# Performance work log

Measured on AMD Instinct MI355X. Metric: run time of the kernel, lower is better.

Reference implementation:

```python
import jax, jax.numpy as jnp
import numpy as np

B, S, D = 2, 2048, 2048
H = 16
NOPE, ROPE, VH = 128, 64, 128
QR, KVR = 512, 512
EPS = 1e-6


def _rmsnorm(x, w):
    return x * jax.lax.rsqrt(jnp.mean(x * x, axis=-1, keepdims=True) + EPS) * w


def _rope(t, freqs_cis):
    # t: (B, h, S, ROPE); freqs_cis: (S, ROPE//2, 2) as (cos, sin)
    b, h, s, d = t.shape
    t2 = t.reshape(b, h, s, d // 2, 2)
    cos = freqs_cis[:, :, 0][None, None]  # (1,1,S,ROPE//2)
    sin = freqs_cis[:, :, 1][None, None]
    x0, x1 = t2[..., 0], t2[..., 1]
    r0 = x0 * cos - x1 * sin
    r1 = x0 * sin + x1 * cos
    return jnp.stack([r0, r1], axis=-1).reshape(b, h, s, d)


def setup_inputs() -> dict:
    key = jax.random.key(0)
    ks = jax.random.split(key, 11)
    def init(k, out_dim, in_dim):
        return jax.random.normal(k, (out_dim, in_dim), jnp.float32) * (1.0 / np.sqrt(in_dim))
    x = jax.random.normal(ks[0], (B, S, D), jnp.float32)
    half = ROPE // 2
    inv = 1.0 / (10000.0 ** (np.arange(half, dtype=np.float64) / half))
    ang = np.outer(np.arange(S), inv)
    freqs_cis = jnp.asarray(np.stack([np.cos(ang), np.sin(ang)], axis=-1), jnp.float32)  # (S, half, 2)
    mask = jnp.ones((S, S), dtype=bool)  # unused (is_causal=True in original)
    return {
        "x": x,
        "mask": mask,
        "freqs_cis": freqs_cis,
        "w_cq": init(ks[1], QR, D),
        "w_qnorm": jnp.ones((QR,), jnp.float32),
        "w_dqn": init(ks[2], H * NOPE, QR),
        "w_dqr": init(ks[3], H * ROPE, QR),
        "w_ckv": init(ks[4], KVR, D),
        "w_kvnorm": jnp.ones((KVR,), jnp.float32),
        "w_dkn": init(ks[5], H * NOPE, KVR),
        "w_dv": init(ks[6], H * VH, KVR),
        "w_krope": init(ks[7], ROPE, D),
        "w_proj": init(ks[8], D, H * VH),
    }


def reference(x, mask, freqs_cis, w_cq, w_qnorm, w_dqn, w_dqr, w_ckv, w_kvnorm, w_dkn, w_dv, w_krope, w_proj):
    b, s, _ = x.shape
    # Q path: compress -> RMSNorm -> decompress (nope, rope)
    cq = jnp.einsum('bsd,rd->bsr', x, w_cq)
    nq = _rmsnorm(cq, w_qnorm)
    q_nope = jnp.einsum('bsr,er->bse', nq, w_dqn).reshape(b, s, H, NOPE).transpose(0, 2, 1, 3)
    q_rope = jnp.einsum('bsr,er->bse', nq, w_dqr).reshape(b, s, H, ROPE).transpose(0, 2, 1, 3)
    # KV path
    ckv = jnp.einsum('bsd,rd->bsr', x, w_ckv)
    nkv = _rmsnorm(ckv, w_kvnorm)
    k_nope = jnp.einsum('bsr,er->bse', nkv, w_dkn).reshape(b, s, H, NOPE).transpose(0, 2, 1, 3)
    value = jnp.einsum('bsr,er->bse', nkv, w_dv).reshape(b, s, H, VH).transpose(0, 2, 1, 3)
    # shared single-head rope key, scaled by 1/num_heads
    k_rope = jnp.einsum('bsd,ed->bse', x, w_krope).reshape(b, s, 1, ROPE).transpose(0, 2, 1, 3) / H
    # partial RoPE
    q_rope = _rope(q_rope, freqs_cis)
    k_rope = _rope(k_rope, freqs_cis)
    # recombine nope|rope
    q = jnp.concatenate([q_nope, q_rope], axis=-1)  # (B,H,S,NOPE+ROPE)
    k = jnp.concatenate([k_nope, jnp.broadcast_to(k_rope, (b, H, s, ROPE))], axis=-1)
    # causal SDPA
    scale = 1.0 / np.sqrt(NOPE + ROPE)
    scores = jnp.einsum('bhqd,bhkd->bhqk', q, k) * scale
    causal = jnp.tril(jnp.ones((s, s), dtype=bool))
    scores = jnp.where(causal[None, None], scores, -jnp.inf)
    attn = jax.nn.softmax(scores, axis=-1)
    out = jnp.einsum('bhqk,bhkv->bhqv', attn, value)  # (B,H,S,VH)
    out = out.transpose(0, 2, 1, 3).reshape(b, s, H * VH)
    return jnp.einsum('bse,de->bsd', out, w_proj)
```

## Files before the change

### kernel.cpp

```cpp
#include <hip/hip_runtime.h>
#include <hip/hip_bf16.h>


typedef __attribute__((ext_vector_type(8))) short s8v;
typedef __attribute__((ext_vector_type(4))) float f4v;

#define DEV static __device__ __forceinline__

DEV ushort f2b(float f) {
  __hip_bfloat16 h = __float2bfloat16(f);
  return *reinterpret_cast<ushort*>(&h);
}
DEV float b2f(ushort u) {
  __hip_bfloat16 h = *reinterpret_cast<__hip_bfloat16*>(&u);
  return __bfloat162float(h);
}
DEV f4v mfma16(s8v a, s8v b, f4v c) {
  return __builtin_amdgcn_mfma_f32_16x16x32_bf16(a, b, c, 0, 0, 0);
}
DEV void gload16(const ushort* g, ushort* l) {
  __builtin_amdgcn_global_load_lds((const __attribute__((address_space(1))) void*)g,
                                   (__attribute__((address_space(3))) void*)l, 16, 0, 0);
}
DEV void barrier_raw() {
  __builtin_amdgcn_sched_barrier(0);
  __builtin_amdgcn_s_barrier();
  __builtin_amdgcn_sched_barrier(0);
}

struct CastSeg { const float* src; ushort* dst; int n4; int blk0; };
struct CastTab { CastSeg seg[10]; };

__global__ __launch_bounds__(256) void cast_all_kernel(CastTab t) {
  int b = blockIdx.x;
  int si = 0;
#pragma unroll
  for (int i = 1; i < 10; ++i) si = (b >= t.seg[i].blk0) ? i : si;
  int i4 = (b - t.seg[si].blk0) * 256 + threadIdx.x;
  if (i4 >= t.seg[si].n4) return;
  ushort4 o;
  if (t.seg[si].src) {
    float4 v = reinterpret_cast<const float4*>(t.seg[si].src)[i4];
    o.x = f2b(v.x); o.y = f2b(v.y); o.z = f2b(v.z); o.w = f2b(v.w);
  } else {
    o = ushort4{0, 0, 0, 0};
  }
  reinterpret_cast<ushort4*>(t.seg[si].dst)[i4] = o;
}

template <bool BF16OUT>
DEV void gemm_core(const ushort* __restrict__ A, const ushort* __restrict__ B,
                   void* __restrict__ C, int N, int K, int row0, int col0,
                   ushort* a_lds0, ushort* a_lds1, ushort* b_lds0, ushort* b_lds1) {
  const int tid = threadIdx.x;
  const int lane = tid & 63, wv = tid >> 6;
  const int wm = wv >> 1, wn = wv & 1;
  const int l15 = lane & 15, l4 = lane >> 4;
  const int srow = lane >> 2;
  const int scol = (lane & 3) * 8;
  ushort* a_lds[2] = {a_lds0, a_lds1};
  ushort* b_lds[2] = {b_lds0, b_lds1};

  f4v acc[4][4];
#pragma unroll
  for (int i = 0; i < 4; ++i)
#pragma unroll
    for (int j = 0; j < 4; ++j) acc[i][j] = f4v{0.f, 0.f, 0.f, 0.f};

  auto stage = [&](int k0, int bsel) {
#pragma unroll
    for (int i = 0; i < 2; ++i) {
      int s = wv * 2 + i;
      gload16(&A[(size_t)(row0 + s * 16 + srow) * K + k0 + scol], &a_lds[bsel][s * 512]);
      gload16(&B[(size_t)(col0 + s * 16 + srow) * K + k0 + scol], &b_lds[bsel][s * 512]);
    }
  };

  stage(0, 0);
  int cur = 0;
  for (int k0 = 0; k0 < K; k0 += 32) {
    __syncthreads();
    if (k0 + 32 < K) stage(k0 + 32, cur ^ 1);
    s8v af[4], bfr[4];
#pragma unroll
    for (int mi = 0; mi < 4; ++mi)
      af[mi] = *reinterpret_cast<const s8v*>(&a_lds[cur][(wm * 64 + mi * 16 + l15) * 32 + 8 * l4]);
#pragma unroll
    for (int ni = 0; ni < 4; ++ni)
      bfr[ni] = *reinterpret_cast<const s8v*>(&b_lds[cur][(wn * 64 + ni * 16 + l15) * 32 + 8 * l4]);
#pragma unroll
    for (int mi = 0; mi < 4; ++mi)
#pragma unroll
      for (int ni = 0; ni < 4; ++ni) acc[mi][ni] = mfma16(af[mi], bfr[ni], acc[mi][ni]);
    cur ^= 1;
  }

#pragma unroll
  for (int mi = 0; mi < 4; ++mi)
#pragma unroll
    for (int ni = 0; ni < 4; ++ni)
#pragma unroll
      for (int j = 0; j < 4; ++j) {
        int r = row0 + wm * 64 + mi * 16 + l4 * 4 + j;
        int cl = col0 + wn * 64 + ni * 16 + l15;
        if (BF16OUT)
          reinterpret_cast<ushort*>(C)[(size_t)r * N + cl] = f2b(acc[mi][ni][j]);
        else
          reinterpret_cast<float*>(C)[(size_t)r * N + cl] = acc[mi][ni][j];
      }
}

template <bool BF16OUT>
__global__ __launch_bounds__(256) void gemm_bt(const ushort* __restrict__ A,
                                               const ushort* __restrict__ B,
                                               void* __restrict__ C, int N, int K) {
  __shared__ ushort a0[128 * 32], a1[128 * 32], b0[128 * 32], b1[128 * 32];
  gemm_core<BF16OUT>(A, B, C, N, K, blockIdx.x * 128, blockIdx.y * 128, a0, a1, b0, b1);
}

__global__ __launch_bounds__(256) void gemm2_dual(const ushort* __restrict__ nq,
                                                  const ushort* __restrict__ w2q,
                                                  ushort* __restrict__ g2q,
                                                  const ushort* __restrict__ nkv,
                                                  const ushort* __restrict__ w2kv,
                                                  ushort* __restrict__ g2kv) {
  __shared__ ushort a0[128 * 32], a1[128 * 32], b0[128 * 32], b1[128 * 32];
  int by = blockIdx.y;
  if (by < 24)
    gemm_core<true>(nq, w2q, g2q, 3072, 512, blockIdx.x * 128, by * 128, a0, a1, b0, b1);
  else
    gemm_core<true>(nkv, w2kv, g2kv, 4096, 512, blockIdx.x * 128, (by - 24) * 128, a0, a1, b0, b1);
}

__global__ __launch_bounds__(256) void norm_rope1_kernel(
    const float* __restrict__ g1, const float* __restrict__ wq, const float* __restrict__ wkv,
    const float* __restrict__ freqs, ushort* __restrict__ nq, ushort* __restrict__ nkv,
    ushort* __restrict__ kro) {
  const int m = blockIdx.x;
  const int s = m & 2047;
  const int tid = threadIdx.x;
  __shared__ float red[4];
  const float* row = g1 + (size_t)m * 1152;

  float v0 = row[tid], v1 = row[tid + 256];
  float ss = v0 * v0 + v1 * v1;
#pragma unroll
  for (int off = 32; off > 0; off >>= 1) ss += __shfl_down(ss, off);
  if ((tid & 63) == 0) red[tid >> 6] = ss;
  __syncthreads();
  float r = rsqrtf((red[0] + red[1] + red[2] + red[3]) * (1.0f / 512.0f) + 1e-6f);
  nq[(size_t)m * 512 + tid] = f2b(v0 * r * wq[tid]);
  nq[(size_t)m * 512 + tid + 256] = f2b(v1 * r * wq[tid + 256]);

  float u0 = row[512 + tid], u1 = row[512 + tid + 256];
  float ss2 = u0 * u0 + u1 * u1;
#pragma unroll
  for (int off = 32; off > 0; off >>= 1) ss2 += __shfl_down(ss2, off);
  __syncthreads();
  if ((tid & 63) == 0) red[tid >> 6] = ss2;
  __syncthreads();
  float r2 = rsqrtf((red[0] + red[1] + red[2] + red[3]) * (1.0f / 512.0f) + 1e-6f);
  nkv[(size_t)m * 512 + tid] = f2b(u0 * r2 * wkv[tid]);
  nkv[(size_t)m * 512 + tid + 256] = f2b(u1 * r2 * wkv[tid + 256]);

  if (tid < 32) {
    float x0 = row[1024 + 2 * tid], x1 = row[1024 + 2 * tid + 1];
    float c = freqs[s * 64 + 2 * tid], sn = freqs[s * 64 + 2 * tid + 1];
    kro[(size_t)m * 64 + 2 * tid] = f2b((x0 * c - x1 * sn) * (1.0f / 16.0f));
    kro[(size_t)m * 64 + 2 * tid + 1] = f2b((x0 * sn + x1 * c) * (1.0f / 16.0f));
  }
}

__global__ __launch_bounds__(256) void misc_fused_kernel(ushort* __restrict__ g2q,
                                                         const float* __restrict__ freqs,
                                                         const ushort* __restrict__ g2kv,
                                                         ushort* __restrict__ vT) {
  const int tid = threadIdx.x;
  if (blockIdx.x < 2048) {
    int blk = blockIdx.x;
    int bh = blk >> 6;
    int rem = blk & 63;
    int st = rem >> 1, dt = rem & 1;
    int b = bh >> 4, h = bh & 15;
    __shared__ ushort t[64][72];
#pragma unroll
    for (int it = 0; it < 2; ++it) {
      int c = tid + it * 256;
      int sl = c >> 3, cc = (c & 7) * 8;
      *reinterpret_cast<uint4*>(&t[sl][cc]) = *reinterpret_cast<const uint4*>(
          &g2kv[(size_t)(b * 2048 + st * 64 + sl) * 4096 + 2048 + h * 128 + dt * 64 + cc]);
    }
    __syncthreads();
#pragma unroll
    for (int it = 0; it < 2; ++it) {
      int c = tid + it * 256;
      int dl = c >> 3, cc = (c & 7) * 8;
      ushort tmp[8];
#pragma unroll
      for (int e = 0; e < 8; ++e) tmp[e] = t[cc + e][dl];
      *reinterpret_cast<uint4*>(&vT[(size_t)(bh * 128 + dt * 64 + dl) * 2048 + st * 64 + cc]) =
          *reinterpret_cast<uint4*>(tmp);
    }
  } else {
    int idx = (blockIdx.x - 2048) * 256 + tid;
    int m = idx >> 9;
    int rem = idx & 511;
    int h = rem >> 5, j = rem & 31;
    int s = m & 2047;
    size_t base = (size_t)m * 3072 + 2048 + h * 64 + 2 * j;
    ushort2 pr = *reinterpret_cast<ushort2*>(&g2q[base]);
    float x0 = b2f(pr.x), x1 = b2f(pr.y);
    float c = freqs[s * 64 + 2 * j], sn = freqs[s * 64 + 2 * j + 1];
    ushort2 o;
    o.x = f2b(x0 * c - x1 * sn);
    o.y = f2b(x0 * sn + x1 * c);
    *reinterpret_cast<ushort2*>(&g2q[base]) = o;
  }
}

__global__ __launch_bounds__(512, 4) void attn_kernel(const ushort* __restrict__ q,
                                                      const ushort* __restrict__ knope,
                                                      const ushort* __restrict__ kro,
                                                      const ushort* __restrict__ vT,
                                                      ushort* __restrict__ out) {
  const int p = blockIdx.x;
  const int a = (p >> 5) & 7;
  const int qt = (p < 256) ? (15 - a) : a;
  const int bh = p & 31;
  const int b = bh >> 4, h = bh & 15;
  const int tid = threadIdx.x, lane = tid & 63, w = tid >> 6;
  const int l15 = lane & 15, l4 = lane >> 4;

  __shared__ ushort kbuf[2][64 * 192];
  __shared__ ushort vbuf[128 * 64];

  s8v qf[6];
  {
    const size_t qbase = (size_t)(b * 2048 + qt * 128 + w * 16 + l15) * 3072;
#pragma unroll
    for (int kc = 0; kc < 4; ++kc)
      qf[kc] = *reinterpret_cast<const s8v*>(&q[qbase + h * 128 + kc * 32 + 8 * l4]);
#pragma unroll
    for (int kc = 4; kc < 6; ++kc)
      qf[kc] = *reinterpret_cast<const s8v*>(&q[qbase + 2048 + h * 64 + (kc - 4) * 32 + 8 * l4]);
  }

  f4v oacc[8];
#pragma unroll
  for (int i = 0; i < 8; ++i) oacc[i] = f4v{0.f, 0.f, 0.f, 0.f};
  float m_r = -INFINITY, l_r = 0.f;
  const float sc2 = 0.07216878364870323f * 1.44269504f;
  const int nkt = 2 * qt + 2;
  const int kbase = b * 2048;
  const int myq = qt * 128 + w * 16 + l15;

  auto stageK = [&](int kt, int bsel) {
    const int krow0 = kbase + kt * 64;
#pragma unroll
    for (int i = 0; i < 3; ++i) {
      int s = w * 3 + i;
      int pp = s * 1024 + lane * 16;
      int row = pp / 384;
      int col = ((pp ^ ((row & 7) << 4)) - row * 384) >> 1;
      const ushort* src = (col < 128)
          ? &knope[(size_t)(krow0 + row) * 4096 + h * 128 + col]
          : &kro[(size_t)(krow0 + row) * 64 + (col - 128)];
      gload16(src, &kbuf[bsel][s * 512]);
    }
  };
  auto stageV = [&](int kt) {
#pragma unroll
    for (int i = 0; i < 2; ++i) {
      int s = w * 2 + i;
      int pp = s * 1024 + lane * 16;
      int d = pp >> 7;
      int key = ((pp ^ ((d & 7) << 4)) & 127) >> 1;
      gload16(&vT[(size_t)(bh * 128 + d) * 2048 + kt * 64 + key], &vbuf[s * 512]);
    }
  };

  stageK(0, 0);
  int cur = 0;
  for (int kt = 0; kt < nkt; ++kt) {
    asm volatile("s_waitcnt vmcnt(0)" ::: "memory");
    barrier_raw();
    stageV(kt);
    if (kt + 1 < nkt) stageK(kt + 1, cur ^ 1);
    const char* kb = (const char*)kbuf[cur];

    f4v sacc[4];
    __builtin_amdgcn_s_setprio(1);
#pragma unroll
    for (int nb = 0; nb < 4; ++nb) {
      sacc[nb] = f4v{0.f, 0.f, 0.f, 0.f};
      const int row = nb * 16 + l15;
      const int sw = (row & 7) << 4;
#pragma unroll
      for (int kc = 0; kc < 6; ++kc) {
        s8v kf = *reinterpret_cast<const s8v*>(kb + row * 384 + ((kc * 64 + l4 * 16) ^ sw));
        sacc[nb] = mfma16(kf, qf[kc], sacc[nb]);
      }
    }
    __builtin_amdgcn_s_setprio(0);

#pragma unroll
    for (int nb = 0; nb < 4; ++nb) {
      int key = kt * 64 + nb * 16 + 4 * l4;
#pragma unroll
      for (int j = 0; j < 4; ++j) {
        float sv = sacc[nb][j] * sc2;
        if (kt >= 2 * qt && key + j > myq) sv = -INFINITY;
        sacc[nb][j] = sv;
      }
    }
    float mx = sacc[0][0];
#pragma unroll
    for (int nb = 0; nb < 4; ++nb)
#pragma unroll
      for (int j = 0; j < 4; ++j) mx = fmaxf(mx, sacc[nb][j]);
    mx = fmaxf(mx, __shfl_xor(mx, 16));
    mx = fmaxf(mx, __shfl_xor(mx, 32));

    if (!__all(mx - m_r <= 8.0f)) {
      float mnew = fmaxf(m_r, mx);
      float al = exp2f(m_r - mnew);
      m_r = mnew;
      l_r *= al;
      float alj[4];
#pragma unroll
      for (int j = 0; j < 4; ++j) alj[j] = __shfl(al, 4 * l4 + j);
#pragma unroll
      for (int nv = 0; nv < 8; ++nv)
#pragma unroll
        for (int j = 0; j < 4; ++j) oacc[nv][j] *= alj[j];
    }
    float rs = 0.f;
#pragma unroll
    for (int nb = 0; nb < 4; ++nb)
#pragma unroll
      for (int j = 0; j < 4; ++j) {
        float pv = exp2f(sacc[nb][j] - m_r);
        sacc[nb][j] = pv;
        rs += pv;
      }
    rs += __shfl_xor(rs, 16);
    rs += __shfl_xor(rs, 32);
    l_r += rs;

    uint pkE[4], pkO[4];
#pragma unroll
    for (int nb = 0; nb < 4; ++nb) {
      pkE[nb] = ((uint)f2b(sacc[nb][1]) << 16) | f2b(sacc[nb][0]);
      pkO[nb] = ((uint)f2b(sacc[nb][3]) << 16) | f2b(sacc[nb][2]);
    }
    const int hi2 = l4 >> 1;
    const int sbase = l15 + 16 * (2 * (l4 & 1));
    union PF { uint u[4]; s8v v; } pf0, pf1;
#pragma unroll
    for (int t = 0; t < 4; ++t) {
      int src = sbase + 16 * (t >> 1);
      uint wa0 = __shfl((t & 1) ? pkO[0] : pkE[0], src);
      uint wb0 = __shfl((t & 1) ? pkO[1] : pkE[1], src);
      pf0.u[t] = hi2 ? wb0 : wa0;
      uint wa1 = __shfl((t & 1) ? pkO[2] : pkE[2], src);
      uint wb1 = __shfl((t & 1) ? pkO[3] : pkE[3], src);
      pf1.u[t] = hi2 ? wb1 : wa1;
    }

    if (kt + 1 < nkt) {
      asm volatile("s_waitcnt vmcnt(3)" ::: "memory");
    } else {
      asm volatile("s_waitcnt vmcnt(0)" ::: "memory");
    }
    barrier_raw();

    const char* vb = (const char*)vbuf;
    __builtin_amdgcn_s_setprio(1);
#pragma unroll
    for (int kc2 = 0; kc2 < 2; ++kc2) {
      s8v pfr = kc2 ? pf1.v : pf0.v;
#pragma unroll
      for (int nv = 0; nv < 8; ++nv) {
        const int d = nv * 16 + l15;
        s8v vf = *reinterpret_cast<const s8v*>(vb + d * 128 + ((kc2 * 64 + l4 * 16) ^ ((d & 7) << 4)));
        oacc[nv] = mfma16(pfr, vf, oacc[nv]);
      }
    }
    __builtin_amdgcn_s_setprio(0);
    cur ^= 1;
  }

  float invl = 1.0f / l_r;
  float invj[4];
#pragma unroll
  for (int j = 0; j < 4; ++j) invj[j] = __shfl(invl, 4 * l4 + j);
#pragma unroll
  for (int j = 0; j < 4; ++j) {
    int m = b * 2048 + qt * 128 + w * 16 + 4 * l4 + j;
#pragma unroll
    for (int nv = 0; nv < 8; ++nv)
      out[(size_t)m * 2048 + h * 128 + nv * 16 + l15] = f2b(oacc[nv][j] * invj[j]);
  }
}

extern "C" void kernel_launch(void* const* d_in, const int* in_sizes, int n_in,
                              void* d_out, int out_size, void* d_ws, size_t ws_size,
                              hipStream_t stream) {
  const float* x       = (const float*)d_in[0];
  const float* freqs   = (const float*)d_in[2];
  const float* w_cq    = (const float*)d_in[3];
  const float* w_qnorm = (const float*)d_in[4];
  const float* w_dqn   = (const float*)d_in[5];
  const float* w_dqr   = (const float*)d_in[6];
  const float* w_ckv   = (const float*)d_in[7];
  const float* w_kvnorm= (const float*)d_in[8];
  const float* w_dkn   = (const float*)d_in[9];
  const float* w_dv    = (const float*)d_in[10];
  const float* w_krope = (const float*)d_in[11];
  const float* w_proj  = (const float*)d_in[12];
  float* out = (float*)d_out;

  char* ws = (char*)d_ws;
  const size_t MB = 1ull << 20;
  ushort* g2kv = (ushort*)(ws + 0);
  float*  g1   = (float*) (ws + 0);
  ushort* g2q  = (ushort*)(ws + 32 * MB);
  ushort* xbf  = (ushort*)(ws + 32 * MB);
  ushort* w1   = (ushort*)(ws + 48 * MB);
  ushort* vT   = (ushort*)(ws + 56 * MB);
  ushort* nq   = (ushort*)(ws + 56 * MB);
  ushort* nkv  = (ushort*)(ws + 60 * MB);
  ushort* w2q  = (ushort*)(ws + 64 * MB);
  ushort* w2kv = (ushort*)(ws + 67 * MB);
  ushort* att  = (ushort*)(ws + 72 * MB);
  ushort* wpj  = (ushort*)(ws + 88 * MB);
  ushort* kro  = (ushort*)(ws + 96 * MB);

  CastTab t;
  const float* srcs[10] = {x, w_cq, w_ckv, w_krope, nullptr,
                           w_dqn, w_dqr, w_dkn, w_dv, w_proj};
  ushort* dsts[10] = {xbf, w1, w1 + 512 * 2048, w1 + 1024 * 2048, w1 + 1088 * 2048,
                      w2q, w2q + 2048 * 512, w2kv, w2kv + 2048 * 512, wpj};
  int ns[10] = {4096 * 2048, 512 * 2048, 512 * 2048, 64 * 2048, 64 * 2048,
                2048 * 512, 1024 * 512, 2048 * 512, 2048 * 512, 2048 * 2048};
  int blk = 0;
  for (int i = 0; i < 10; ++i) {
    t.seg[i].src = srcs[i];
    t.seg[i].dst = dsts[i];
    t.seg[i].n4 = ns[i] / 4;
    t.seg[i].blk0 = blk;
    blk += (ns[i] / 4 + 255) / 256;
  }
  cast_all_kernel<<<blk, 256, 0, stream>>>(t);

  gemm_bt<false><<<dim3(32, 9), 256, 0, stream>>>(xbf, w1, g1, 1152, 2048);
  norm_rope1_kernel<<<4096, 256, 0, stream>>>(g1, w_qnorm, w_kvnorm, freqs, nq, nkv, kro);
  gemm2_dual<<<dim3(32, 56), 256, 0, stream>>>(nq, w2q, g2q, nkv, w2kv, g2kv);
  misc_fused_kernel<<<2048 + 8192, 256, 0, stream>>>(g2q, freqs, g2kv, vT);
  attn_kernel<<<512, 512, 0, stream>>>(g2q, g2kv, kro, vT, att);
  gemm_bt<false><<<dim3(32, 16), 256, 0, stream>>>(att, wpj, out, 2048, 2048);
}
```

Measured before the change: 461.8 us.

## Balance causal attention work by splitting heavy query tiles across blocks with merge

Each block now processes exactly 17 KV tiles. It pairs a heavy query tile (8+pi) with a light one (7-pi), and the heavy tile's KV range is split between two blocks that write partial O/m/l, which a new merge kernel combines. V staging is also double-buffered, which removes the mid-iteration barrier. The aim is to remove the load imbalance from causal masking and the extra sync per tile. The cost is fp32 partial traffic (kept in the output buffer as scratch), an extra kernel launch, and more shared memory.

Result: no change. 468.0 us (+1.3%).

```diff
diff --git a/kernel.cpp b/kernel.cpp
--- a/kernel.cpp
+++ b/kernel.cpp
@@ -218,24 +218,35 @@
   }
 }
 
+#define MINIT -3.0e4f
 __global__ __launch_bounds__(512, 4) void attn_kernel(const ushort* __restrict__ q,
                                                       const ushort* __restrict__ knope,
                                                       const ushort* __restrict__ kro,
                                                       const ushort* __restrict__ vT,
-                                                      ushort* __restrict__ out) {
-  const int p = blockIdx.x;
-  const int a = (p >> 5) & 7;
-  const int qt = (p < 256) ? (15 - a) : a;
-  const int bh = p & 31;
+                                                      ushort* __restrict__ out,
+                                                      float* __restrict__ opart,
+                                                      float* __restrict__ mlbuf) {
+  const int g = blockIdx.x;
+  const int pi = g >> 6;
+  const int half = (g >> 5) & 1;
+  const int bh = g & 31;
+  const int qt_h = 8 + pi, qt_l = 7 - pi;
   const int b = bh >> 4, h = bh & 15;
   const int tid = threadIdx.x, lane = tid & 63, w = tid >> 6;
   const int l15 = lane & 15, l4 = lane >> 4;
 
   __shared__ ushort kbuf[2][64 * 192];
-  __shared__ ushort vbuf[128 * 64];
+  __shared__ ushort vbuf[2][128 * 64];
+
+  const int n1 = half ? (2 * qt_h - 15) : 17;
+  const int kvA0 = half ? 17 : 0;
+  const int NJ = 17;
+
+  auto jobQt = [&](int i) { return (i < n1) ? qt_h : qt_l; };
+  auto jobKv = [&](int i) { return (i < n1) ? (kvA0 + i) : (i - n1); };
 
   s8v qf[6];
-  {
+  auto loadQ = [&](int qt) {
     const size_t qbase = (size_t)(b * 2048 + qt * 128 + w * 16 + l15) * 3072;
 #pragma unroll
     for (int kc = 0; kc < 4; ++kc)
@@ -243,19 +254,21 @@
 #pragma unroll
     for (int kc = 4; kc < 6; ++kc)
       qf[kc] = *reinterpret_cast<const s8v*>(&q[qbase + 2048 + h * 64 + (kc - 4) * 32 + 8 * l4]);
-  }
+  };
 
   f4v oacc[8];
-#pragma unroll
-  for (int i = 0; i < 8; ++i) oacc[i] = f4v{0.f, 0.f, 0.f, 0.f};
-  float m_r = -INFINITY, l_r = 0.f;
+  float m_r, l_r;
+  auto resetS = [&]() {
+#pragma unroll
+    for (int i = 0; i < 8; ++i) oacc[i] = f4v{0.f, 0.f, 0.f, 0.f};
+    m_r = MINIT; l_r = 0.f;
+  };
+
   const float sc2 = 0.07216878364870323f * 1.44269504f;
-  const int nkt = 2 * qt + 2;
   const int kbase = b * 2048;
-  const int myq = qt * 128 + w * 16 + l15;
-
-  auto stageK = [&](int kt, int bsel) {
-    const int krow0 = kbase + kt * 64;
+
+  auto stageK = [&](int kv, int bsel) {
+    const int krow0 = kbase + kv * 64;
 #pragma unroll
     for (int i = 0; i < 3; ++i) {
       int s = w * 3 + i;
@@ -268,25 +281,64 @@
       gload16(src, &kbuf[bsel][s * 512]);
     }
   };
-  auto stageV = [&](int kt) {
+  auto stageV = [&](int kv, int bsel) {
 #pragma unroll
     for (int i = 0; i < 2; ++i) {
       int s = w * 2 + i;
       int pp = s * 1024 + lane * 16;
       int d = pp >> 7;
       int key = ((pp ^ ((d & 7) << 4)) & 127) >> 1;
-      gload16(&vT[(size_t)(bh * 128 + d) * 2048 + kt * 64 + key], &vbuf[s * 512]);
-    }
-  };
-
-  stageK(0, 0);
-  int cur = 0;
-  for (int kt = 0; kt < nkt; ++kt) {
+      gload16(&vT[(size_t)(bh * 128 + d) * 2048 + kv * 64 + key], &vbuf[bsel][s * 512]);
+    }
+  };
+
+  auto writePartial = [&](int part) {
+    float* Op = opart + (((size_t)(pi * 32 + bh) * 2 + part) << 14);
+#pragma unroll
+    for (int j = 0; j < 4; ++j)
+#pragma unroll
+      for (int nv = 0; nv < 8; ++nv)
+        Op[(w * 16 + 4 * l4 + j) * 128 + nv * 16 + l15] = oacc[nv][j];
+    if (l4 == 0) {
+      float* mlp = mlbuf + ((pi * 32 + bh) * 2 + part) * 256 + (w * 16 + l15) * 2;
+      mlp[0] = m_r; mlp[1] = l_r;
+    }
+  };
+  auto writeFinal = [&](int qt) {
+    float invl = 1.0f / l_r;
+    float invj[4];
+#pragma unroll
+    for (int j = 0; j < 4; ++j) invj[j] = __shfl(invl, 4 * l4 + j);
+#pragma unroll
+    for (int j = 0; j < 4; ++j) {
+      int m = b * 2048 + qt * 128 + w * 16 + 4 * l4 + j;
+#pragma unroll
+      for (int nv = 0; nv < 8; ++nv)
+        out[(size_t)m * 2048 + h * 128 + nv * 16 + l15] = f2b(oacc[nv][j] * invj[j]);
+    }
+  };
+
+  loadQ(jobQt(0));
+  resetS();
+  stageK(jobKv(0), 0);
+  stageV(jobKv(0), 0);
+
+  for (int i = 0; i < NJ; ++i) {
     asm volatile("s_waitcnt vmcnt(0)" ::: "memory");
     barrier_raw();
-    stageV(kt);
-    if (kt + 1 < nkt) stageK(kt + 1, cur ^ 1);
-    const char* kb = (const char*)kbuf[cur];
+    if (i + 1 < NJ) {
+      stageV(jobKv(i + 1), (i + 1) & 1);
+      stageK(jobKv(i + 1), (i + 1) & 1);
+    }
+    if (half && i == n1) {
+      writePartial(1);
+      resetS();
+      loadQ(qt_l);
+    }
+    const int qt = jobQt(i), kv = jobKv(i);
+    const int myq = qt * 128 + w * 16 + l15;
+    const char* kb = (const char*)kbuf[i & 1];
+    const char* vb = (const char*)vbuf[i & 1];
 
     f4v sacc[4];
     __builtin_amdgcn_s_setprio(1);
@@ -305,11 +357,11 @@
 
 #pragma unroll
     for (int nb = 0; nb < 4; ++nb) {
-      int key = kt * 64 + nb * 16 + 4 * l4;
+      int key = kv * 64 + nb * 16 + 4 * l4;
 #pragma unroll
       for (int j = 0; j < 4; ++j) {
         float sv = sacc[nb][j] * sc2;
-        if (kt >= 2 * qt && key + j > myq) sv = -INFINITY;
+        if (kv >= 2 * qt && key + j > myq) sv = -INFINITY;
         sacc[nb][j] = sv;
       }
     }
@@ -367,14 +419,6 @@
       pf1.u[t] = hi2 ? wb1 : wa1;
     }
 
-    if (kt + 1 < nkt) {
-      asm volatile("s_waitcnt vmcnt(3)" ::: "memory");
-    } else {
-      asm volatile("s_waitcnt vmcnt(0)" ::: "memory");
-    }
-    barrier_raw();
-
-    const char* vb = (const char*)vbuf;
     __builtin_amdgcn_s_setprio(1);
 #pragma unroll
     for (int kc2 = 0; kc2 < 2; ++kc2) {
@@ -387,19 +431,41 @@
       }
     }
     __builtin_amdgcn_s_setprio(0);
-    cur ^= 1;
-  }
-
-  float invl = 1.0f / l_r;
-  float invj[4];
-#pragma unroll
-  for (int j = 0; j < 4; ++j) invj[j] = __shfl(invl, 4 * l4 + j);
-#pragma unroll
-  for (int j = 0; j < 4; ++j) {
-    int m = b * 2048 + qt * 128 + w * 16 + 4 * l4 + j;
-#pragma unroll
-    for (int nv = 0; nv < 8; ++nv)
-      out[(size_t)m * 2048 + h * 128 + nv * 16 + l15] = f2b(oacc[nv][j] * invj[j]);
+  }
+
+  if (half == 0) writePartial(0);
+  else writeFinal(qt_l);
+}
+
+__global__ __launch_bounds__(256) void merge_kernel(const float* __restrict__ opart,
+                                                    const float* __restrict__ mlbuf,
+                                                    ushort* __restrict__ att) {
+  const int g = blockIdx.x;
+  const int pi = g >> 5, bh = g & 31;
+  const int qt = 8 + pi, b = bh >> 4, h = bh & 15;
+  const int t = threadIdx.x;
+  const int r = t >> 1, c0 = (t & 1) * 64;
+
+  const int pb = (pi * 32 + bh) * 2;
+  float m0 = mlbuf[pb * 256 + r * 2], l0 = mlbuf[pb * 256 + r * 2 + 1];
+  float m1 = mlbuf[(pb + 1) * 256 + r * 2], l1 = mlbuf[(pb + 1) * 256 + r * 2 + 1];
+  float m = fmaxf(m0, m1);
+  float a0 = exp2f(m0 - m), a1 = exp2f(m1 - m);
+  float inv = 1.0f / (l0 * a0 + l1 * a1);
+
+  const float* O0 = opart + ((size_t)pb << 14) + r * 128 + c0;
+  const float* O1 = opart + ((size_t)(pb + 1) << 14) + r * 128 + c0;
+  ushort* dst = att + (size_t)(b * 2048 + qt * 128 + r) * 2048 + h * 128 + c0;
+#pragma unroll
+  for (int d = 0; d < 64; d += 4) {
+    float4 v0 = *reinterpret_cast<const float4*>(O0 + d);
+    float4 v1 = *reinterpret_cast<const float4*>(O1 + d);
+    ushort4 o;
+    o.x = f2b((v0.x * a0 + v1.x * a1) * inv);
+    o.y = f2b((v0.y * a0 + v1.y * a1) * inv);
+    o.z = f2b((v0.z * a0 + v1.z * a1) * inv);
+    o.w = f2b((v0.w * a0 + v1.w * a1) * inv);
+    *reinterpret_cast<ushort4*>(dst + d) = o;
   }
 }
 
@@ -435,6 +501,8 @@
   ushort* att  = (ushort*)(ws + 72 * MB);
   ushort* wpj  = (ushort*)(ws + 88 * MB);
   ushort* kro  = (ushort*)(ws + 96 * MB);
+  float*  mlb  = (float*) (ws + 97 * MB);
+  float*  opart= out;
 
   CastTab t;
   const float* srcs[10] = {x, w_cq, w_ckv, w_krope, nullptr,
@@ -457,6 +525,7 @@
   norm_rope1_kernel<<<4096, 256, 0, stream>>>(g1, w_qnorm, w_kvnorm, freqs, nq, nkv, kro);
   gemm2_dual<<<dim3(32, 56), 256, 0, stream>>>(nq, w2q, g2q, nkv, w2kv, g2kv);
   misc_fused_kernel<<<2048 + 8192, 256, 0, stream>>>(g2q, freqs, g2kv, vT);
-  attn_kernel<<<512, 512, 0, stream>>>(g2q, g2kv, kro, vT, att);
+  attn_kernel<<<512, 512, 0, stream>>>(g2q, g2kv, kro, vT, att, opart, mlb);
+  merge_kernel<<<256, 256, 0, stream>>>(opart, mlb, att);
   gemm_bt<false><<<dim3(32, 16), 256, 0, stream>>>(att, wpj, out, 2048, 2048);
 }
```
